# Kernel tuning notes

Hardware: AMD Instinct MI355X
Metric: run time of the kernel (lower is better)

The kernel has to match this reference:

```python
import jax, jax.numpy as jnp
import numpy as np

# ---- static config (mirrors cfg) ----
B, N, K = 2, 8192, 40
FIRST_DL = 0.03
CONV_RADIUS = 2.5
DEFORM_RADIUS = 5.0
ARCH = ['simple', 'resnetb', 'resnetb_strided', 'resnetb', 'resnetb_strided', 'resnetb', 'nearest_upsample']
SENTINEL = N  # out-of-range support index (torch code uses N_spts_total; here per-batch padded slot count)
GRID = 4096   # voxel hash multiplier; coords stay < GRID for pts in [0,1], dl >= 0.06


def _ball_query_one(q, s, qmask, smask, radius):
    """Radius ball-query: K nearest supports within radius. q:[N,3] s:[M,3]."""
    d2 = jnp.sum((q[:, None, :] - s[None, :, :]) ** 2, axis=-1)          # [N,M]
    d2 = jnp.where(smask[None, :] & (d2 <= radius * radius), d2, jnp.inf)
    vals, idx = jax.lax.top_k(-d2, K)                                     # [N,K]
    idx = jnp.where(jnp.isfinite(vals) & qmask[:, None], idx, SENTINEL)
    return idx.astype(jnp.int32)


ball_query = jax.vmap(_ball_query_one, in_axes=(0, 0, 0, 0, None))


def _grid_subsample_one(pts, mask, dl):
    """Voxel-grid subsampling with unweighted average (padded to N rows)."""
    INT_MAX = jnp.iinfo(jnp.int32).max
    c = jnp.floor(pts / dl).astype(jnp.int32)                             # nonneg for pts in [0,1]
    key_v = (c[:, 0] * GRID + c[:, 1]) * GRID + c[:, 2]
    key_v = jnp.where(mask, key_v, INT_MAX)
    order = jnp.argsort(key_v)
    sk = key_v[order]
    sp = pts[order]
    new = jnp.concatenate([jnp.ones((1,), bool), sk[1:] != sk[:-1]])
    seg = jnp.cumsum(new) - 1                                             # segment id per sorted point
    sums = jax.ops.segment_sum(sp, seg, num_segments=N)                   # [N,3]
    cnt = jax.ops.segment_sum(jnp.ones((N,), pts.dtype), seg, num_segments=N)
    segkey = jax.ops.segment_max(sk, seg, num_segments=N)
    valid = (cnt > 0) & (segkey != INT_MAX)                               # invalid pads sort last
    means = jnp.where(valid[:, None], sums / jnp.maximum(cnt, 1.0)[:, None], 0.0)
    return means, valid, jnp.sum(valid).astype(jnp.int32)


grid_subsample = jax.vmap(_grid_subsample_one, in_axes=(0, 0, None))


def setup_inputs() -> dict:
    key = jax.random.key(0)
    pts = jax.random.uniform(key, (B, N, 3), dtype=jnp.float32)
    return {"pts": pts}


def reference(pts):
    pmask = jnp.ones((B, N), bool)
    lengths = jnp.full((B,), N, jnp.int32)
    points = pts
    r_normal = FIRST_DL * CONV_RADIUS
    layer_blocks = []
    out_points, out_neigh, out_pool, out_up, out_len = [], [], [], [], []
    for bi, block in enumerate(ARCH):
        if 'global' in block or 'upsample' in block:
            break
        if not ('pool' in block or 'strided' in block):
            layer_blocks.append(block)
            if bi < len(ARCH) - 1 and 'upsample' not in ARCH[bi + 1]:
                continue
        if layer_blocks:
            if any('deformable' in b for b in layer_blocks[:-1]):
                r = r_normal * DEFORM_RADIUS / CONV_RADIUS
            else:
                r = r_normal
            conv_i = ball_query(points, points, pmask, pmask, r)
        else:
            conv_i = jnp.full((B, N, K), SENTINEL, jnp.int32)
        if 'pool' in block or 'strided' in block:
            dl = 2 * r_normal / CONV_RADIUS
            pool_p, pool_m, pool_len = grid_subsample(points, pmask, dl)
            r = r_normal * DEFORM_RADIUS / CONV_RADIUS if 'deformable' in block else r_normal
            pool_i = ball_query(pool_p, points, pool_m, pmask, r)
            up_i = ball_query(points, pool_p, pmask, pool_m, 2 * r)
        else:
            pool_i = jnp.full((B, N, K), SENTINEL, jnp.int32)
            up_i = jnp.full((B, N, K), SENTINEL, jnp.int32)
            pool_p = jnp.zeros((B, N, 3), points.dtype)
            pool_m = jnp.zeros((B, N), bool)
            pool_len = jnp.zeros((B,), jnp.int32)
        out_points.append(points)
        out_neigh.append(conv_i)
        out_pool.append(pool_i)
        out_up.append(up_i)
        out_len.append(lengths)
        points, pmask, lengths = pool_p, pool_m, pool_len
        r_normal *= 2
        layer_blocks = []
    return (jnp.stack(out_points),   # [L,B,N,3] padded points per layer
            jnp.stack(out_neigh),    # [L,B,N,K] conv neighbor indices
            jnp.stack(out_pool),     # [L,B,N,K] pooling indices
            jnp.stack(out_up),       # [L,B,N,K] upsampling indices
            jnp.stack(out_len))      # [L,B]     valid lengths
```

## Files before the change

kernel.cpp:

```cpp
#include <hip/hip_runtime.h>

#define BB   2
#define NN   8192
#define KNN  40
#define SENT 8192
#define G0   17
#define G1   9
#define G0_3 (G0*G0*G0)
#define G1_3 (G1*G1*G1)

#define GA   13
#define GB   6
#define GC   3
#define GA_3 (GA*GA*GA)
#define GB_3 (GB*GB*GB)
#define GC_3 (GC*GC*GC)

typedef unsigned long long ull;
typedef unsigned int       u32;
typedef unsigned short     u16;

__device__ __forceinline__ float sqdist(float qx, float qy, float qz,
                                        float sx, float sy, float sz) {
    float dx = __fsub_rn(qx, sx);
    float dy = __fsub_rn(qy, sy);
    float dz = __fsub_rn(qz, sz);
    return __fadd_rn(__fadd_rn(__fmul_rn(dx, dx), __fmul_rn(dy, dy)),
                     __fmul_rn(dz, dz));
}

__device__ __forceinline__ int cell1(float p, float Gf, int G) {
    int c = (int)floorf(__fmul_rn(p, Gf));
    return min(max(c, 0), G - 1);
}
__device__ __forceinline__ int vcell1(float p, float dlf, int G) {
    int c = (int)floorf(__fdiv_rn(p, dlf));
    return min(max(c, 0), G - 1);
}

__device__ __forceinline__ ull shfl_u64(ull x, int src) {
    int lo = __shfl((int)(u32)x, src);
    int hi = __shfl((int)(u32)(x >> 32), src);
    return ((ull)(u32)hi << 32) | (ull)(u32)lo;
}
__device__ __forceinline__ ull shflxor_u64(ull x, int m) {
    int lo = __shfl_xor((int)(u32)x, m);
    int hi = __shfl_xor((int)(u32)(x >> 32), m);
    return ((ull)(u32)hi << 32) | (ull)(u32)lo;
}

__global__ void prep_kernel(const float* __restrict__ pts, float* __restrict__ dout) {
    const size_t PN = (size_t)BB * NN * 3;
    const size_t IN = (size_t)BB * NN * KNN;
    float* out_points0 = dout;
    float* out_pool2   = dout + 3 * PN + 3 * IN + 2 * IN;
    float* out_up2     = dout + 3 * PN + 6 * IN + 2 * IN;
    float* out_len     = dout + 3 * PN + 9 * IN;
    int i = blockIdx.x * 256 + threadIdx.x;
    if (i < (int)PN) out_points0[i] = pts[i];
    if (i < (int)IN) {
        out_pool2[i] = (float)SENT;
        out_up2[i]   = (float)SENT;
    }
    if (i == 0) { out_len[0] = (float)NN; out_len[1] = (float)NN; }
}

__global__ __launch_bounds__(1024) void csr_build(
    const float* __restrict__ pts, const int* __restrict__ len_ptr, int len_const,
    int G, int G3, int* __restrict__ off, int* __restrict__ lst,
    float dlfv, int Gv, int G3v, int* __restrict__ offv, int* __restrict__ rankv,
    int* __restrict__ lstv, int* __restrict__ lenv_dev, float* __restrict__ lenv_out_f) {
    __shared__ int scnt[GA_3];
    __shared__ int soff[GA_3];
    __shared__ int svcnt[G0_3];
    __shared__ int svoff[G0_3];
    __shared__ int wsum[16];
    int b = blockIdx.x;
    int t = threadIdx.x;
    int len = len_ptr ? len_ptr[b] : len_const;
    const float* pb = pts + (size_t)b * NN * 3;
    float Gf = (float)G;
    bool dosub = Gv > 0;
    for (int v = t; v < G3; v += 1024) scnt[v] = 0;
    if (dosub) for (int v = t; v < G3v; v += 1024) svcnt[v] = 0;
    __syncthreads();
    for (int i = t; i < len; i += 1024) {
        float px = pb[i * 3], py = pb[i * 3 + 1], pz = pb[i * 3 + 2];
        int c = (cell1(px, Gf, G) * G + cell1(py, Gf, G)) * G + cell1(pz, Gf, G);
        atomicAdd(&scnt[c], 1);
        if (dosub) {
            int cv = (vcell1(px, dlfv, Gv) * Gv + vcell1(py, dlfv, Gv)) * Gv
                     + vcell1(pz, dlfv, Gv);
            atomicAdd(&svcnt[cv], 1);
        }
    }
    __syncthreads();
    int lane = t & 63, wid = t >> 6;
    {
        int per = (G3 + 1023) >> 10;
        int start = t * per, end = min(start + per, G3);
        if (start > G3) start = G3;
        int csum = 0;
        for (int v = start; v < end; ++v) csum += scnt[v];
        int inc = csum;
        for (int d = 1; d < 64; d <<= 1) {
            int u = __shfl_up(inc, d);
            if (lane >= d) inc += u;
        }
        if (lane == 63) wsum[wid] = inc;
        __syncthreads();
        if (t < 16) {
            int wv = wsum[t];
            for (int d = 1; d < 16; d <<= 1) {
                int u = __shfl_up(wv, d);
                if (t >= d) wv += u;
            }
            wsum[t] = wv;
        }
        __syncthreads();
        int excl = inc - csum + (wid ? wsum[wid - 1] : 0);
        int run = excl;
        int* offb = off + (size_t)b * (G3 + 1);
        for (int v = start; v < end; ++v) {
            soff[v] = run;
            offb[v] = run;
            run += scnt[v];
        }
        if (t == 0) offb[G3] = len;
    }
    __syncthreads();
    if (dosub) {
        int per = (G3v + 1023) >> 10;
        int start = t * per, end = min(start + per, G3v);
        if (start > G3v) start = G3v;
        int ce = 0, co = 0;
        for (int v = start; v < end; ++v) { ce += svcnt[v]; co += (svcnt[v] > 0); }
        int pack = (ce << 14) | co;
        int inc = pack;
        for (int d = 1; d < 64; d <<= 1) {
            int u = __shfl_up(inc, d);
            if (lane >= d) inc += u;
        }
        if (lane == 63) wsum[wid] = inc;
        __syncthreads();
        if (t < 16) {
            int wv = wsum[t];
            for (int d = 1; d < 16; d <<= 1) {
                int u = __shfl_up(wv, d);
                if (t >= d) wv += u;
            }
            wsum[t] = wv;
        }
        __syncthreads();
        int excl = inc - pack + (wid ? wsum[wid - 1] : 0);
        int rune = excl >> 14;
        int runo = excl & 16383;
        int total = wsum[15] & 16383;
        int* offvb  = offv  + (size_t)b * (G3v + 1);
        int* rankvb = rankv + (size_t)b * G3v;
        for (int v = start; v < end; ++v) {
            svoff[v]  = rune;
            offvb[v]  = rune;
            rankvb[v] = runo;
            rune += svcnt[v];
            runo += (svcnt[v] > 0);
        }
        if (t == 0) {
            offvb[G3v] = len;
            lenv_dev[b] = total;
            lenv_out_f[b] = (float)total;
        }
    }
    __syncthreads();
    for (int v = t; v < G3; v += 1024) scnt[v] = 0;
    if (dosub) for (int v = t; v < G3v; v += 1024) svcnt[v] = 0;
    __syncthreads();
    int* lstb = lst + (size_t)b * NN;
    int* lstvb = dosub ? (lstv + (size_t)b * NN) : nullptr;
    for (int i = t; i < len; i += 1024) {
        float px = pb[i * 3], py = pb[i * 3 + 1], pz = pb[i * 3 + 2];
        int c = (cell1(px, Gf, G) * G + cell1(py, Gf, G)) * G + cell1(pz, Gf, G);
        int pos = soff[c] + atomicAdd(&scnt[c], 1);
        lstb[pos] = i;
        if (dosub) {
            int cv = (vcell1(px, dlfv, Gv) * Gv + vcell1(py, dlfv, Gv)) * Gv
                     + vcell1(pz, dlfv, Gv);
            int posv = svoff[cv] + atomicAdd(&svcnt[cv], 1);
            lstvb[posv] = i;
        }
    }
}

__global__ __launch_bounds__(256) void sub_means(
    const float* __restrict__ pts, const int* __restrict__ offg,
    const int* __restrict__ rankg, const int* __restrict__ lst,
    const int* __restrict__ len_dev, int G3, float* __restrict__ out_pts) {
    int b = blockIdx.y;
    int i = blockIdx.x * 256 + threadIdx.x;
    const float* pb = pts + (size_t)b * NN * 3;
    const int* offb  = offg + (size_t)b * (G3 + 1);
    const int* lstb  = lst + (size_t)b * NN;
    if (i < G3) {
        int s = offb[i], e = offb[i + 1];
        int cn = e - s;
        if (cn > 0) {
            float sx = 0.f, sy = 0.f, sz = 0.f;
            int last = -1;
            for (int k = 0; k < cn; ++k) {
                int m = 0x7FFFFFFF;
                for (int j = s; j < e; ++j) {
                    int idx = lstb[j];
                    if (idx > last && idx < m) m = idx;
                }
                sx = __fadd_rn(sx, pb[m * 3]);
                sy = __fadd_rn(sy, pb[m * 3 + 1]);
                sz = __fadd_rn(sz, pb[m * 3 + 2]);
                last = m;
            }
            float rinv = __frcp_rn((float)cn);
            int rk = rankg[(size_t)b * G3 + i];
            float* op = out_pts + ((size_t)b * NN + rk) * 3;
            op[0] = __fmul_rn(sx, rinv);
            op[1] = __fmul_rn(sy, rinv);
            op[2] = __fmul_rn(sz, rinv);
        }
    }
    int total = len_dev[b];
    if (i >= total && i < NN) {
        float* op = out_pts + ((size_t)b * NN + i) * 3;
        op[0] = 0.f; op[1] = 0.f; op[2] = 0.f;
    }
}

__global__ __launch_bounds__(256) void bq_wave2(
    const float* __restrict__ qA, const int* __restrict__ qlApt, int qlAc,
    const float* __restrict__ sA, const int* __restrict__ offAp,
    const int* __restrict__ lstAp, int GpA, int G3pA, float r2A,
    float* __restrict__ outA,
    const float* __restrict__ qB, const int* __restrict__ qlBpt, int qlBc,
    const float* __restrict__ sB, const int* __restrict__ offBp,
    const int* __restrict__ lstBp, int GpB, int G3pB, float r2B,
    float* __restrict__ outB) {
    const ull INITK = ~0ull;
    int z = blockIdx.z;
    const float* qpts = z ? qB : qA;
    const int* qlen_ptr = z ? qlBpt : qlApt;
    int qlen_const = z ? qlBc : qlAc;
    const float* spts = z ? sB : sA;
    const int* off = z ? offBp : offAp;
    const int* lst = z ? lstBp : lstAp;
    int G  = z ? GpB : GpA;
    int G3 = z ? G3pB : G3pA;
    float r2 = z ? r2B : r2A;
    float* out = z ? outB : outA;

    int t = threadIdx.x;
    int lane = t & 63;
    int b = blockIdx.y;
    int qi = blockIdx.x * 4 + (t >> 6);
    int qlen = qlen_ptr ? qlen_ptr[b] : qlen_const;
    float* op = out + ((size_t)b * NN + qi) * KNN;
    if (qi >= qlen) {
        if (lane < KNN) op[lane] = (float)SENT;
        return;
    }
    const float* qp = qpts + ((size_t)b * NN + qi) * 3;
    float qx = qp[0], qy = qp[1], qz = qp[2];
    float Gf = (float)G;
    int cx = cell1(qx, Gf, G), cy = cell1(qy, Gf, G), cz = cell1(qz, Gf, G);
    const int* offb = off + (size_t)b * (G3 + 1);
    const int* lstb = lst + (size_t)b * NN;
    const float* sp = spts + (size_t)b * NN * 3;

    int cnt = 0, cst = 0;
    if (lane < 27) {
        int dz = lane % 3 - 1, dy = (lane / 3) % 3 - 1, dxx = lane / 9 - 1;
        int x = cx + dxx, y = cy + dy, zz = cz + dz;
        bool ok = ((unsigned)x < (unsigned)G) & ((unsigned)y < (unsigned)G)
                                              & ((unsigned)zz < (unsigned)G);
        int c = ok ? (x * G + y) * G + zz : 0;
        int s = ok ? offb[c] : 0;
        int e = ok ? offb[c + 1] : 0;
        cnt = e - s;
        cst = s;
    }
    int incl = cnt;
#pragma unroll
    for (int d_ = 1; d_ < 64; d_ <<= 1) {
        int u = __shfl_up(incl, d_);
        if (lane >= d_) incl += u;
    }
    int excl = incl - cnt;
    int T = __shfl(incl, 63);

    ull res = INITK;
    bool have_res = false;
    for (int r0 = 0; r0 < T; r0 += 512) {
        ull c0 = INITK, c1 = INITK, c2 = INITK, c3 = INITK,
            c4 = INITK, c5 = INITK, c6 = INITK, c7 = INITK;
#define FILL(S, CS) if (r0 + (S) * 64 < T) {                                   \
            int g = r0 + (S) * 64 + lane;                                      \
            bool gok = g < T;                                                  \
            int gc = gok ? g : (T - 1);                                        \
            int d = 0;                                                         \
            if (__shfl(excl, d | 16) <= gc) d |= 16;                           \
            if (__shfl(excl, d | 8)  <= gc) d |= 8;                            \
            if (__shfl(excl, d | 4)  <= gc) d |= 4;                            \
            if (__shfl(excl, d | 2)  <= gc) d |= 2;                            \
            if (__shfl(excl, d | 1)  <= gc) d |= 1;                            \
            int st = __shfl(cst, d), eg = __shfl(excl, d);                     \
            int idx = lstb[st + (gc - eg)];                                    \
            float sx = sp[idx * 3], sy = sp[idx * 3 + 1], sz = sp[idx * 3 + 2];\
            float d2 = sqdist(qx, qy, qz, sx, sy, sz);                         \
            if (gok && d2 <= r2)                                               \
                CS = (((ull)__float_as_uint(d2)) << 13) | (ull)(u32)idx;       \
        }
        FILL(0, c0) FILL(1, c1) FILL(2, c2) FILL(3, c3)
        FILL(4, c4) FILL(5, c5) FILL(6, c6) FILL(7, c7)
#undef FILL
#define CE(A, B) { ull lo_ = (A < B) ? A : B; ull hi_ = (A < B) ? B : A; A = lo_; B = hi_; }
        CE(c0,c1) CE(c2,c3) CE(c4,c5) CE(c6,c7)
        CE(c0,c2) CE(c1,c3) CE(c4,c6) CE(c5,c7)
        CE(c1,c2) CE(c5,c6)
        CE(c0,c4) CE(c1,c5) CE(c2,c6) CE(c3,c7)
        CE(c2,c4) CE(c3,c5)
        CE(c1,c2) CE(c3,c4) CE(c5,c6)
#undef CE
        int m = (c0 != INITK) + (c1 != INITK) + (c2 != INITK) + (c3 != INITK)
              + (c4 != INITK) + (c5 != INITK) + (c6 != INITK) + (c7 != INITK);
        int incm = m;
#pragma unroll
        for (int d_ = 1; d_ < 64; d_ <<= 1) {
            int u = __shfl_up(incm, d_);
            if (lane >= d_) incm += u;
        }
        int base = incm - m;
        int M = __shfl(incm, 63);
        int npass = (M + 63) >> 6;
        for (int p = 0; p < npass; ++p) {
            int D = p * 64 + lane;
            bool dok = D < M;
            int Dc = dok ? D : (M - 1);
            int l = 0;
            if (__shfl(base, l | 32) <= Dc) l |= 32;
            if (__shfl(base, l | 16) <= Dc) l |= 16;
            if (__shfl(base, l | 8)  <= Dc) l |= 8;
            if (__shfl(base, l | 4)  <= Dc) l |= 4;
            if (__shfl(base, l | 2)  <= Dc) l |= 2;
            if (__shfl(base, l | 1)  <= Dc) l |= 1;
            int j = Dc - __shfl(base, l);
            ull p0 = shfl_u64(c0, l), p1 = shfl_u64(c1, l);
            ull p2 = shfl_u64(c2, l), p3 = shfl_u64(c3, l);
            ull p4 = shfl_u64(c4, l), p5 = shfl_u64(c5, l);
            ull p6 = shfl_u64(c6, l), p7 = shfl_u64(c7, l);
            ull a0 = (j & 1) ? p1 : p0;
            ull a1 = (j & 1) ? p3 : p2;
            ull a2 = (j & 1) ? p5 : p4;
            ull a3 = (j & 1) ? p7 : p6;
            ull b0 = (j & 2) ? a1 : a0;
            ull b1 = (j & 2) ? a3 : a2;
            ull key = (j & 4) ? b1 : b0;
            if (!dok) key = INITK;
#pragma unroll
            for (int k = 2; k <= 64; k <<= 1) {
#pragma unroll
                for (int jj = k >> 1; jj > 0; jj >>= 1) {
                    ull other = shflxor_u64(key, jj);
                    bool up = ((lane & k) == 0);
                    bool lowlane = ((lane & jj) == 0);
                    bool takeMin = (lowlane == up);
                    bool lt = key < other;
                    key = (takeMin == lt) ? key : other;
                }
            }
            if (!have_res) {
                res = key;
                have_res = true;
            } else {
                ull rb = shfl_u64(key, 63 - lane);
                ull lo_ = (res < rb) ? res : rb;
#pragma unroll
                for (int jj = 32; jj > 0; jj >>= 1) {
                    ull other = shflxor_u64(lo_, jj);
                    bool lowlane = ((lane & jj) == 0);
                    bool lt = lo_ < other;
                    lo_ = (lowlane == lt) ? lo_ : other;
                }
                res = lo_;
            }
        }
    }
    if (lane < KNN)
        op[lane] = (res == INITK) ? (float)SENT : (float)(int)(res & 0x1FFFu);
}

extern "C" void kernel_launch(void* const* d_in, const int* in_sizes, int n_in,
                              void* d_out, int out_size, void* d_ws, size_t ws_size,
                              hipStream_t stream) {
    const float* pts = (const float*)d_in[0];
    float* dout = (float*)d_out;
    const size_t PN = (size_t)BB * NN * 3;
    const size_t IN = (size_t)BB * NN * KNN;
    float* out_points = dout;
    float* out_neigh  = dout + 3 * PN;
    float* out_pool   = out_neigh + 3 * IN;
    float* out_up     = out_pool + 3 * IN;
    float* out_len    = out_up + 3 * IN;
    float* pts1 = out_points + PN;
    float* pts2 = out_points + 2 * PN;

    int*   len1  = (int*)d_ws;
    int*   len2  = len1 + BB;
    int*   offV0 = len2 + BB;
    int*   rnk0  = offV0 + (size_t)BB * (G0_3 + 1);
    int*   lstV0 = rnk0 + (size_t)BB * G0_3;
    int*   offV1 = lstV0 + (size_t)BB * NN;
    int*   rnk1  = offV1 + (size_t)BB * (G1_3 + 1);
    int*   lstV1 = rnk1 + (size_t)BB * G1_3;
    int*   offA  = lstV1 + (size_t)BB * NN;
    int*   lstA  = offA + (size_t)BB * (GA_3 + 1);
    int*   offB  = lstA + (size_t)BB * NN;
    int*   lstB  = offB + (size_t)BB * (GB_3 + 1);
    int*   offC  = lstB + (size_t)BB * NN;
    int*   lstC  = offC + (size_t)BB * (GC_3 + 1);

    double r_normal = 0.03 * 2.5;
    double r0 = r_normal;
    double dl0 = 2.0 * r_normal / 2.5;
    float r2_0   = (float)(r0 * r0);
    float r2_up0 = (float)((2.0 * r0) * (2.0 * r0));
    float dlf0   = (float)dl0;
    r_normal *= 2.0;
    double r1 = r_normal;
    double dl1 = 2.0 * r_normal / 2.5;
    float r2_1   = (float)(r1 * r1);
    float r2_up1 = (float)((2.0 * r1) * (2.0 * r1));
    float dlf1   = (float)dl1;
    r_normal *= 2.0;
    float r2_2 = (float)(r_normal * r_normal);

    dim3 qgrid1(NN / 4, BB, 1);
    dim3 qgrid2(NN / 4, BB, 2);
    dim3 mgrid(NN / 256, BB);

    prep_kernel<<<(int)((IN + 255) / 256), 256, 0, stream>>>(pts, dout);
    csr_build<<<BB, 1024, 0, stream>>>(pts, nullptr, NN, GA, GA_3, offA, lstA,
                                       dlf0, G0, G0_3, offV0, rnk0, lstV0,
                                       len1, out_len + 2);
    sub_means<<<mgrid, 256, 0, stream>>>(pts, offV0, rnk0, lstV0, len1, G0_3, pts1);
    bq_wave2<<<qgrid1, 256, 0, stream>>>(
        pts, nullptr, NN, pts, offA, lstA, GA, GA_3, r2_0, out_neigh + 0 * IN,
        pts, nullptr, NN, pts, offA, lstA, GA, GA_3, r2_0, out_neigh + 0 * IN);
    csr_build<<<BB, 1024, 0, stream>>>(pts1, len1, 0, GB, GB_3, offB, lstB,
                                       dlf1, G1, G1_3, offV1, rnk1, lstV1,
                                       len2, out_len + 4);
    sub_means<<<mgrid, 256, 0, stream>>>(pts1, offV1, rnk1, lstV1, len2, G1_3, pts2);
    bq_wave2<<<qgrid2, 256, 0, stream>>>(
        pts1, len1, 0, pts, offA, lstA, GA, GA_3, r2_0, out_pool + 0 * IN,
        pts, nullptr, NN, pts1, offB, lstB, GB, GB_3, r2_up0, out_up + 0 * IN);
    bq_wave2<<<qgrid2, 256, 0, stream>>>(
        pts1, len1, 0, pts1, offB, lstB, GB, GB_3, r2_1, out_neigh + 1 * IN,
        pts2, len2, 0, pts1, offB, lstB, GB, GB_3, r2_1, out_pool + 1 * IN);
    csr_build<<<BB, 1024, 0, stream>>>(pts2, len2, 0, GC, GC_3, offC, lstC,
                                       0.f, 0, 0, nullptr, nullptr, nullptr,
                                       nullptr, nullptr);
    bq_wave2<<<qgrid2, 256, 0, stream>>>(
        pts1, len1, 0, pts2, offC, lstC, GC, GC_3, r2_up1, out_up + 1 * IN,
        pts2, len2, 0, pts2, offC, lstC, GC, GC_3, r2_2, out_neigh + 2 * IN);
}
```

Measured before the change: 218.6 us.

## Fuse subsample means into CSR build and batch ball queries into two launches

The voxel-mean subsampling kernel is folded into the start of the next level's CSR build, so each level's points are produced by the same single block that then bins them. All seven ball queries are deferred until after the three CSR builds and issued as two launches with up to four query sets per grid. This cuts kernel launches and serialization points. Inside the query kernel, candidate keys are now compacted through a per-wave LDS buffer instead of a binary search plus eight 64-bit shuffles and selects. The trade-off is that the mean computation now runs inside only BB blocks of 1024 threads instead of a wide grid, which adds serial work to the critical path before the queries can start.

```diff
diff --git a/kernel.cpp b/kernel.cpp
--- a/kernel.cpp
+++ b/kernel.cpp
@@ -66,10 +66,14 @@
 }
 
 __global__ __launch_bounds__(1024) void csr_build(
-    const float* __restrict__ pts, const int* __restrict__ len_ptr, int len_const,
+    const float* pts, float* pts_w,
+    const int* __restrict__ len_ptr, int len_const,
     int G, int G3, int* __restrict__ off, int* __restrict__ lst,
     float dlfv, int Gv, int G3v, int* __restrict__ offv, int* __restrict__ rankv,
-    int* __restrict__ lstv, int* __restrict__ lenv_dev, float* __restrict__ lenv_out_f) {
+    int* __restrict__ lstv, int* __restrict__ lenv_dev, float* __restrict__ lenv_out_f,
+    const float* __restrict__ msrc, const int* __restrict__ moff,
+    const int* __restrict__ mrnk, const int* __restrict__ mlst,
+    const int* __restrict__ mlen_dev, int mG3) {
     __shared__ int scnt[GA_3];
     __shared__ int soff[GA_3];
     __shared__ int svcnt[G0_3];
@@ -77,6 +81,44 @@
     __shared__ int wsum[16];
     int b = blockIdx.x;
     int t = threadIdx.x;
+    if (pts_w) {
+        const float* mb = msrc + (size_t)b * NN * 3;
+        const int* mob = moff + (size_t)b * (mG3 + 1);
+        const int* mlb = mlst + (size_t)b * NN;
+        for (int i = t; i < mG3; i += 1024) {
+            int s = mob[i], e = mob[i + 1];
+            int cn = e - s;
+            if (cn > 0) {
+                float sx = 0.f, sy = 0.f, sz = 0.f;
+                int last = -1;
+                for (int k = 0; k < cn; ++k) {
+                    int m = 0x7FFFFFFF;
+                    for (int j = s; j < e; ++j) {
+                        int idx = mlb[j];
+                        if (idx > last && idx < m) m = idx;
+                    }
+                    sx = __fadd_rn(sx, mb[m * 3]);
+                    sy = __fadd_rn(sy, mb[m * 3 + 1]);
+                    sz = __fadd_rn(sz, mb[m * 3 + 2]);
+                    last = m;
+                }
+                float rinv = __frcp_rn((float)cn);
+                int rk = mrnk[(size_t)b * mG3 + i];
+                float* op = pts_w + ((size_t)b * NN + rk) * 3;
+                op[0] = __fmul_rn(sx, rinv);
+                op[1] = __fmul_rn(sy, rinv);
+                op[2] = __fmul_rn(sz, rinv);
+            }
+        }
+        int total = mlen_dev[b];
+        for (int r = t; r < NN; r += 1024) {
+            if (r >= total) {
+                float* op = pts_w + ((size_t)b * NN + r) * 3;
+                op[0] = 0.f; op[1] = 0.f; op[2] = 0.f;
+            }
+        }
+        __syncthreads();
+    }
     int len = len_ptr ? len_ptr[b] : len_const;
     const float* pb = pts + (size_t)b * NN * 3;
     float Gf = (float)G;
@@ -191,71 +233,31 @@
     }
 }
 
-__global__ __launch_bounds__(256) void sub_means(
-    const float* __restrict__ pts, const int* __restrict__ offg,
-    const int* __restrict__ rankg, const int* __restrict__ lst,
-    const int* __restrict__ len_dev, int G3, float* __restrict__ out_pts) {
-    int b = blockIdx.y;
-    int i = blockIdx.x * 256 + threadIdx.x;
-    const float* pb = pts + (size_t)b * NN * 3;
-    const int* offb  = offg + (size_t)b * (G3 + 1);
-    const int* lstb  = lst + (size_t)b * NN;
-    if (i < G3) {
-        int s = offb[i], e = offb[i + 1];
-        int cn = e - s;
-        if (cn > 0) {
-            float sx = 0.f, sy = 0.f, sz = 0.f;
-            int last = -1;
-            for (int k = 0; k < cn; ++k) {
-                int m = 0x7FFFFFFF;
-                for (int j = s; j < e; ++j) {
-                    int idx = lstb[j];
-                    if (idx > last && idx < m) m = idx;
-                }
-                sx = __fadd_rn(sx, pb[m * 3]);
-                sy = __fadd_rn(sy, pb[m * 3 + 1]);
-                sz = __fadd_rn(sz, pb[m * 3 + 2]);
-                last = m;
-            }
-            float rinv = __frcp_rn((float)cn);
-            int rk = rankg[(size_t)b * G3 + i];
-            float* op = out_pts + ((size_t)b * NN + rk) * 3;
-            op[0] = __fmul_rn(sx, rinv);
-            op[1] = __fmul_rn(sy, rinv);
-            op[2] = __fmul_rn(sz, rinv);
-        }
-    }
-    int total = len_dev[b];
-    if (i >= total && i < NN) {
-        float* op = out_pts + ((size_t)b * NN + i) * 3;
-        op[0] = 0.f; op[1] = 0.f; op[2] = 0.f;
-    }
-}
-
-__global__ __launch_bounds__(256) void bq_wave2(
-    const float* __restrict__ qA, const int* __restrict__ qlApt, int qlAc,
-    const float* __restrict__ sA, const int* __restrict__ offAp,
-    const int* __restrict__ lstAp, int GpA, int G3pA, float r2A,
-    float* __restrict__ outA,
-    const float* __restrict__ qB, const int* __restrict__ qlBpt, int qlBc,
-    const float* __restrict__ sB, const int* __restrict__ offBp,
-    const int* __restrict__ lstBp, int GpB, int G3pB, float r2B,
-    float* __restrict__ outB) {
+struct BqArgs {
+    const float* q; const int* qlp; int qlc;
+    const float* s; const int* off; const int* lst;
+    int G; int G3; float r2; float* out;
+};
+
+__global__ __launch_bounds__(256) void bq_wave4(BqArgs pA, BqArgs pB,
+                                                BqArgs pC, BqArgs pD) {
     const ull INITK = ~0ull;
+    __shared__ ull wlds[4][512];
     int z = blockIdx.z;
-    const float* qpts = z ? qB : qA;
-    const int* qlen_ptr = z ? qlBpt : qlApt;
-    int qlen_const = z ? qlBc : qlAc;
-    const float* spts = z ? sB : sA;
-    const int* off = z ? offBp : offAp;
-    const int* lst = z ? lstBp : lstAp;
-    int G  = z ? GpB : GpA;
-    int G3 = z ? G3pB : G3pA;
-    float r2 = z ? r2B : r2A;
-    float* out = z ? outB : outA;
+    const float* qpts   = z == 0 ? pA.q   : (z == 1 ? pB.q   : (z == 2 ? pC.q   : pD.q));
+    const int* qlen_ptr = z == 0 ? pA.qlp : (z == 1 ? pB.qlp : (z == 2 ? pC.qlp : pD.qlp));
+    int qlen_const      = z == 0 ? pA.qlc : (z == 1 ? pB.qlc : (z == 2 ? pC.qlc : pD.qlc));
+    const float* spts   = z == 0 ? pA.s   : (z == 1 ? pB.s   : (z == 2 ? pC.s   : pD.s));
+    const int* off      = z == 0 ? pA.off : (z == 1 ? pB.off : (z == 2 ? pC.off : pD.off));
+    const int* lst      = z == 0 ? pA.lst : (z == 1 ? pB.lst : (z == 2 ? pC.lst : pD.lst));
+    int G               = z == 0 ? pA.G   : (z == 1 ? pB.G   : (z == 2 ? pC.G   : pD.G));
+    int G3              = z == 0 ? pA.G3  : (z == 1 ? pB.G3  : (z == 2 ? pC.G3  : pD.G3));
+    float r2            = z == 0 ? pA.r2  : (z == 1 ? pB.r2  : (z == 2 ? pC.r2  : pD.r2));
+    float* out          = z == 0 ? pA.out : (z == 1 ? pB.out : (z == 2 ? pC.out : pD.out));
 
     int t = threadIdx.x;
     int lane = t & 63;
+    ull* wl = wlds[t >> 6];
     int b = blockIdx.y;
     int qi = blockIdx.x * 4 + (t >> 6);
     int qlen = qlen_ptr ? qlen_ptr[b] : qlen_const;
@@ -304,7 +306,7 @@
             int gc = gok ? g : (T - 1);                                        \
             int d = 0;                                                         \
             if (__shfl(excl, d | 16) <= gc) d |= 16;                           \
-            if (__shfl(excl, d | 8)  <= gc) d |= 8;                            \
+            if (__shfl(excl, d | 8)  <= gc) d |= 8;                           \
             if (__shfl(excl, d | 4)  <= gc) d |= 4;                            \
             if (__shfl(excl, d | 2)  <= gc) d |= 2;                            \
             if (__shfl(excl, d | 1)  <= gc) d |= 1;                            \
@@ -336,31 +338,24 @@
         }
         int base = incm - m;
         int M = __shfl(incm, 63);
+        asm volatile("s_waitcnt lgkmcnt(0)" ::: "memory");
+        __builtin_amdgcn_sched_barrier(0);
+        if (m > 0) {
+            wl[base] = c0;
+            if (m > 1) wl[base + 1] = c1;
+            if (m > 2) wl[base + 2] = c2;
+            if (m > 3) wl[base + 3] = c3;
+            if (m > 4) wl[base + 4] = c4;
+            if (m > 5) wl[base + 5] = c5;
+            if (m > 6) wl[base + 6] = c6;
+            if (m > 7) wl[base + 7] = c7;
+        }
+        asm volatile("s_waitcnt lgkmcnt(0)" ::: "memory");
+        __builtin_amdgcn_sched_barrier(0);
         int npass = (M + 63) >> 6;
         for (int p = 0; p < npass; ++p) {
             int D = p * 64 + lane;
-            bool dok = D < M;
-            int Dc = dok ? D : (M - 1);
-            int l = 0;
-            if (__shfl(base, l | 32) <= Dc) l |= 32;
-            if (__shfl(base, l | 16) <= Dc) l |= 16;
-            if (__shfl(base, l | 8)  <= Dc) l |= 8;
-            if (__shfl(base, l | 4)  <= Dc) l |= 4;
-            if (__shfl(base, l | 2)  <= Dc) l |= 2;
-            if (__shfl(base, l | 1)  <= Dc) l |= 1;
-            int j = Dc - __shfl(base, l);
-            ull p0 = shfl_u64(c0, l), p1 = shfl_u64(c1, l);
-            ull p2 = shfl_u64(c2, l), p3 = shfl_u64(c3, l);
-            ull p4 = shfl_u64(c4, l), p5 = shfl_u64(c5, l);
-            ull p6 = shfl_u64(c6, l), p7 = shfl_u64(c7, l);
-            ull a0 = (j & 1) ? p1 : p0;
-            ull a1 = (j & 1) ? p3 : p2;
-            ull a2 = (j & 1) ? p5 : p4;
-            ull a3 = (j & 1) ? p7 : p6;
-            ull b0 = (j & 2) ? a1 : a0;
-            ull b1 = (j & 2) ? a3 : a2;
-            ull key = (j & 4) ? b1 : b0;
-            if (!dok) key = INITK;
+            ull key = (D < M) ? wl[D] : INITK;
 #pragma unroll
             for (int k = 2; k <= 64; k <<= 1) {
 #pragma unroll
@@ -439,32 +434,31 @@
     r_normal *= 2.0;
     float r2_2 = (float)(r_normal * r_normal);
 
-    dim3 qgrid1(NN / 4, BB, 1);
-    dim3 qgrid2(NN / 4, BB, 2);
-    dim3 mgrid(NN / 256, BB);
+    BqArgs conv0 = { pts,  nullptr, NN, pts,  offA, lstA, GA, GA_3, r2_0,   out_neigh + 0 * IN };
+    BqArgs pool0 = { pts1, len1,    0,  pts,  offA, lstA, GA, GA_3, r2_0,   out_pool  + 0 * IN };
+    BqArgs up0   = { pts,  nullptr, NN, pts1, offB, lstB, GB, GB_3, r2_up0, out_up    + 0 * IN };
+    BqArgs conv1 = { pts1, len1,    0,  pts1, offB, lstB, GB, GB_3, r2_1,   out_neigh + 1 * IN };
+    BqArgs pool1 = { pts2, len2,    0,  pts1, offB, lstB, GB, GB_3, r2_1,   out_pool  + 1 * IN };
+    BqArgs up1   = { pts1, len1,    0,  pts2, offC, lstC, GC, GC_3, r2_up1, out_up    + 1 * IN };
+    BqArgs conv2 = { pts2, len2,    0,  pts2, offC, lstC, GC, GC_3, r2_2,   out_neigh + 2 * IN };
+
+    dim3 qgrid3(NN / 4, BB, 3);
+    dim3 qgrid4(NN / 4, BB, 4);
 
     prep_kernel<<<(int)((IN + 255) / 256), 256, 0, stream>>>(pts, dout);
-    csr_build<<<BB, 1024, 0, stream>>>(pts, nullptr, NN, GA, GA_3, offA, lstA,
-                                       dlf0, G0, G0_3, offV0, rnk0, lstV0,
-                                       len1, out_len + 2);
-    sub_means<<<mgrid, 256, 0, stream>>>(pts, offV0, rnk0, lstV0, len1, G0_3, pts1);
-    bq_wave2<<<qgrid1, 256, 0, stream>>>(
-        pts, nullptr, NN, pts, offA, lstA, GA, GA_3, r2_0, out_neigh + 0 * IN,
-        pts, nullptr, NN, pts, offA, lstA, GA, GA_3, r2_0, out_neigh + 0 * IN);
-    csr_build<<<BB, 1024, 0, stream>>>(pts1, len1, 0, GB, GB_3, offB, lstB,
-                                       dlf1, G1, G1_3, offV1, rnk1, lstV1,
-                                       len2, out_len + 4);
-    sub_means<<<mgrid, 256, 0, stream>>>(pts1, offV1, rnk1, lstV1, len2, G1_3, pts2);
-    bq_wave2<<<qgrid2, 256, 0, stream>>>(
-        pts1, len1, 0, pts, offA, lstA, GA, GA_3, r2_0, out_pool + 0 * IN,
-        pts, nullptr, NN, pts1, offB, lstB, GB, GB_3, r2_up0, out_up + 0 * IN);
-    bq_wave2<<<qgrid2, 256, 0, stream>>>(
-        pts1, len1, 0, pts1, offB, lstB, GB, GB_3, r2_1, out_neigh + 1 * IN,
-        pts2, len2, 0, pts1, offB, lstB, GB, GB_3, r2_1, out_pool + 1 * IN);
-    csr_build<<<BB, 1024, 0, stream>>>(pts2, len2, 0, GC, GC_3, offC, lstC,
-                                       0.f, 0, 0, nullptr, nullptr, nullptr,
-                                       nullptr, nullptr);
-    bq_wave2<<<qgrid2, 256, 0, stream>>>(
-        pts1, len1, 0, pts2, offC, lstC, GC, GC_3, r2_up1, out_up + 1 * IN,
-        pts2, len2, 0, pts2, offC, lstC, GC, GC_3, r2_2, out_neigh + 2 * IN);
-}
+    csr_build<<<BB, 1024, 0, stream>>>(pts, nullptr, nullptr, NN, GA, GA_3,
+                                       offA, lstA, dlf0, G0, G0_3, offV0, rnk0,
+                                       lstV0, len1, out_len + 2,
+                                       nullptr, nullptr, nullptr, nullptr,
+                                       nullptr, 0);
+    csr_build<<<BB, 1024, 0, stream>>>(pts1, pts1, len1, 0, GB, GB_3,
+                                       offB, lstB, dlf1, G1, G1_3, offV1, rnk1,
+                                       lstV1, len2, out_len + 4,
+                                       pts, offV0, rnk0, lstV0, len1, G0_3);
+    csr_build<<<BB, 1024, 0, stream>>>(pts2, pts2, len2, 0, GC, GC_3,
+                                       offC, lstC, 0.f, 0, 0, nullptr, nullptr,
+                                       nullptr, nullptr, nullptr,
+                                       pts1, offV1, rnk1, lstV1, len2, G1_3);
+    bq_wave4<<<qgrid3, 256, 0, stream>>>(conv0, pool0, up0, up0);
+    bq_wave4<<<qgrid4, 256, 0, stream>>>(conv1, pool1, up1, conv2);
+}
```

Measured after the change: 226.7 us. +3.7%, slower.
